# Kernel optimization log

Hardware: AMD Instinct MI355X
Metric: run time of the kernel (lower is better)

Reference implementation:

```python
import jax, jax.numpy as jnp
import numpy as np

N = 50000   # nodes
E = 800000  # directed edges (self loops added in reference)
F = 8       # temporal features
D = 64      # hidden_channels
H = 4       # heads
C = D // H  # per-head channels = 16
L = 3       # num GAT layers
T = 3       # node types
TE = 16     # type embed dim


def _glorot(key, shape):
    fan_in, fan_out = shape[-2], shape[-1]
    s = jnp.sqrt(6.0 / (fan_in + fan_out))
    return jax.random.uniform(key, shape, jnp.float32, -s, s)


def setup_inputs() -> dict:
    key = jax.random.key(0)
    ks = jax.random.split(key, 24)
    return {
        'x': jax.random.normal(ks[0], (N, F), jnp.float32),
        'node_type': jax.random.randint(ks[1], (N,), 0, T),
        'edge_src': jax.random.randint(ks[2], (E,), 0, N),
        'edge_dst': jax.random.randint(ks[3], (E,), 0, N),
        # TemporalEncoder (Linear F->D + ReLU)
        'Wt': _glorot(ks[4], (F, D)), 'bt': jnp.zeros((D,), jnp.float32),
        # type embedding and input projection
        'Et': 0.1 * jax.random.normal(ks[5], (T, TE), jnp.float32),
        'Wp': _glorot(ks[6], (D + TE, D)), 'bp': jnp.zeros((D,), jnp.float32),
        # GATv2 layers (stacked over L)
        'Wl': _glorot(ks[7], (L, D, H * C)), 'bl': jnp.zeros((L, H * C), jnp.float32),
        'Wr': _glorot(ks[8], (L, D, H * C)), 'br': jnp.zeros((L, H * C), jnp.float32),
        'att': _glorot(ks[9], (L, H, C)),
        'Wres': _glorot(ks[10], (L, D, H * C)),
        'bconv': jnp.zeros((L, H * C), jnp.float32),
        'gamma': jnp.ones((L, D), jnp.float32), 'beta': jnp.zeros((L, D), jnp.float32),
        'alpha': jnp.float32(0.5),
        # output head
        'W1': _glorot(ks[11], (D, D // 2)), 'b1': jnp.zeros((D // 2,), jnp.float32),
        'W2': _glorot(ks[12], (D // 2, 1)), 'b2': jnp.zeros((1,), jnp.float32),
    }


def _layernorm(x, g, b, eps=1e-5):
    mu = jnp.mean(x, -1, keepdims=True)
    v = jnp.mean((x - mu) ** 2, -1, keepdims=True)
    return g * (x - mu) / jnp.sqrt(v + eps) + b


def reference(x, node_type, edge_src, edge_dst, Wt, bt, Et, Wp, bp,
              Wl, bl, Wr, br, att, Wres, bconv, gamma, beta, alpha,
              W1, b1, W2, b2):
    # temporal encoder + type embedding + input projection
    h = jax.nn.relu(x @ Wt + bt)                       # [N, D]
    h = jnp.concatenate([h, Et[node_type]], axis=-1) @ Wp + bp
    h0 = h

    # add self loops once (eval mode -> no dropout)
    loop = jnp.arange(N)
    src = jnp.concatenate([edge_src, loop])            # [E']
    dst = jnp.concatenate([edge_dst, loop])

    for l in range(L):
        xl = (h @ Wl[l] + bl[l]).reshape(N, H, C)      # source transform
        xr = (h @ Wr[l] + br[l]).reshape(N, H, C)      # target transform
        e = jax.nn.leaky_relu(xl[src] + xr[dst], 0.2)  # [E', H, C]
        score = jnp.einsum('ehc,hc->eh', e, att[l])    # [E', H]
        # segment softmax over incoming edges of each destination node
        m = jax.ops.segment_max(score, dst, num_segments=N)
        ex = jnp.exp(score - m[dst])
        s = jax.ops.segment_sum(ex, dst, num_segments=N)
        a = ex / (s[dst] + 1e-16)                      # [E', H]
        msg = xl[src] * a[:, :, None]                  # [E', H, C]
        out = jax.ops.segment_sum(msg, dst, num_segments=N).reshape(N, H * C)
        out = out + h @ Wres[l] + bconv[l]             # GATv2 residual + bias
        h = _layernorm(alpha * out + (1.0 - alpha) * h0, gamma[l], beta[l])

    z = jax.nn.relu(h @ W1 + b1)
    return jax.nn.sigmoid(z @ W2 + b2)                 # [N, 1]
```

## Files before the change

### kernel.cpp

```cpp
#include <hip/hip_runtime.h>
#include <hip/hip_bf16.h>

typedef __hip_bfloat16 bf16;
typedef __attribute__((ext_vector_type(8))) short short8;
typedef __attribute__((ext_vector_type(4))) float f32x4;

__device__ __forceinline__ float b2f(bf16 v) { return __bfloat162float(v); }
__device__ __forceinline__ bf16 f2b(float v) { return __float2bfloat16(v); }
__device__ __forceinline__ short f2bs(float v) {
    bf16 b = f2b(v);
    return *reinterpret_cast<short*>(&b);
}
__device__ __forceinline__ float bflo(unsigned int u) { return __uint_as_float(u << 16); }
__device__ __forceinline__ float bfhi(unsigned int u) { return __uint_as_float(u & 0xffff0000u); }
__device__ __forceinline__ unsigned int packbf(float lo, float hi) {
    bf16 l = f2b(lo), h = f2b(hi);
    return ((unsigned int)(*(unsigned short*)&h) << 16) | (*(unsigned short*)&l);
}


__global__ void k_sentinel(float* out, int n, float val) {
    int i = blockIdx.x * blockDim.x + threadIdx.x;
    if (i < n) out[i] = val;
}

__global__ void k_prep(const float* __restrict__ Wl, const float* __restrict__ Wr,
                       const float* __restrict__ Wres, const float* __restrict__ Wp,
                       const float* __restrict__ W1, const float* __restrict__ Et,
                       const float* __restrict__ bp,
                       bf16* __restrict__ WT, bf16* __restrict__ WpT,
                       bf16* __restrict__ W1T, float* __restrict__ TyB,
                       int* __restrict__ counts, int n) {
    int i = blockIdx.x * 256 + threadIdx.x;
    if (i < n) counts[i] = 0;
    if (i < 36864) {
        int l = i / 12288, rem = i % 12288;
        int col = rem / 64, k = rem % 64;
        int mat = col >> 6, c = col & 63;
        const float* W = (mat == 0) ? Wl : (mat == 1) ? Wr : Wres;
        WT[i] = f2b(W[l * 4096 + k * 64 + c]);
    } else if (i < 40960) {
        int j = i - 36864, col = j / 64, k = j % 64;
        WpT[j] = f2b(Wp[k * 64 + col]);
    } else if (i < 43008) {
        int j = i - 40960, col = j / 64, k = j % 64;
        W1T[j] = f2b(W1[k * 32 + col]);
    } else if (i < 43200) {
        int j = i - 43008, t = j / 64, d = j % 64;
        float s = bp[d];
#pragma unroll
        for (int f = 0; f < 16; ++f) s += Et[t * 16 + f] * Wp[(64 + f) * 64 + d];
        TyB[j] = s;
    }
}

__global__ __launch_bounds__(256) void k_enc_mfma(
        const float* __restrict__ x, const int* __restrict__ ntype,
        const float* __restrict__ Wt, const float* __restrict__ bt,
        const bf16* __restrict__ WpT, const float* __restrict__ TyB,
        float* __restrict__ h0, bf16* __restrict__ hbf, int n) {
    __shared__ float sWt[512];
    __shared__ float sbt[64];
    int tid = threadIdx.x;
    for (int i = tid; i < 512; i += 256) sWt[i] = Wt[i];
    if (tid < 64) sbt[tid] = bt[tid];
    __syncthreads();
    int wave = tid >> 6, lane = tid & 63;
    int nb = blockIdx.x * 64 + wave * 16;
    if (nb >= n) return;
    int m = lane & 15, q = lane >> 4;

    const float* xrow = x + (size_t)(nb + m) * 8;
    float xv[8];
#pragma unroll
    for (int f = 0; f < 8; ++f) xv[f] = xrow[f];

    short8 a0, a1;
#pragma unroll
    for (int j = 0; j < 8; ++j) {
        int c0 = q * 8 + j, c1 = 32 + q * 8 + j;
        float s0 = sbt[c0], s1 = sbt[c1];
#pragma unroll
        for (int f = 0; f < 8; ++f) {
            s0 += xv[f] * sWt[f * 64 + c0];
            s1 += xv[f] * sWt[f * 64 + c1];
        }
        a0[j] = f2bs(fmaxf(s0, 0.f));
        a1[j] = f2bs(fmaxf(s1, 0.f));
    }

    int ty[4];
#pragma unroll
    for (int r = 0; r < 4; ++r) ty[r] = ntype[nb + q * 4 + r];

#pragma unroll
    for (int t = 0; t < 4; ++t) {
        const short* wp = (const short*)(WpT + (size_t)(t * 16 + m) * 64) + q * 8;
        short8 b0 = *(const short8*)(wp);
        short8 b1 = *(const short8*)(wp + 32);
        f32x4 acc = {0.f, 0.f, 0.f, 0.f};
        acc = __builtin_amdgcn_mfma_f32_16x16x32_bf16(a0, b0, acc, 0, 0, 0);
        acc = __builtin_amdgcn_mfma_f32_16x16x32_bf16(a1, b1, acc, 0, 0, 0);
        int col = t * 16 + m;
#pragma unroll
        for (int r = 0; r < 4; ++r) {
            int nd = nb + q * 4 + r;
            float val = acc[r] + TyB[ty[r] * 64 + col];
            h0[(size_t)nd * 64 + col] = val;
            hbf[(size_t)nd * 64 + col] = f2b(val);
        }
    }
}

__global__ void k_count(const int* __restrict__ dst, int* __restrict__ counts,
                        int* __restrict__ rank, int e) {
    int i = blockIdx.x * blockDim.x + threadIdx.x;
    if (i < e) rank[i] = atomicAdd(&counts[dst[i]], 1);
}

__global__ void k_scan_local(const int* __restrict__ counts, int* __restrict__ row_raw,
                             int* __restrict__ bsum, int n) {
    __shared__ int part[256];
    int tid = threadIdx.x;
    int base = blockIdx.x * 1024 + tid * 4;
    int c0 = (base     < n) ? counts[base]     + 1 : 0;
    int c1 = (base + 1 < n) ? counts[base + 1] + 1 : 0;
    int c2 = (base + 2 < n) ? counts[base + 2] + 1 : 0;
    int c3 = (base + 3 < n) ? counts[base + 3] + 1 : 0;
    part[tid] = c0 + c1 + c2 + c3;
    __syncthreads();
    for (int off = 1; off < 256; off <<= 1) {
        int t = (tid >= off) ? part[tid - off] : 0;
        __syncthreads();
        part[tid] += t;
        __syncthreads();
    }
    int ex = (tid == 0) ? 0 : part[tid - 1];
    if (base     < n) row_raw[base]     = ex;
    if (base + 1 < n) row_raw[base + 1] = ex + c0;
    if (base + 2 < n) row_raw[base + 2] = ex + c0 + c1;
    if (base + 3 < n) row_raw[base + 3] = ex + c0 + c1 + c2;
    if (tid == 255) bsum[blockIdx.x] = part[255];
}

__global__ void k_scan_bsum(int* __restrict__ bsum, int* __restrict__ row_ptr,
                            int g, int n) {
    int lane = threadIdx.x;
    int orig = (lane < g) ? bsum[lane] : 0;
    int v = orig;
#pragma unroll
    for (int off = 1; off < 64; off <<= 1) {
        int t = __shfl_up(v, off, 64);
        if (lane >= off) v += t;
    }
    if (lane < g) bsum[lane] = v - orig;
    if (lane == 63) row_ptr[n] = v;
}

__global__ void k_build(const int* __restrict__ src, const int* __restrict__ dst,
                        const int* __restrict__ row_raw, const int* __restrict__ bsum,
                        const int* __restrict__ rank,
                        int* __restrict__ row_ptr, int* __restrict__ csr_src,
                        int n, int e) {
    int i = blockIdx.x * 256 + threadIdx.x;
    if (i < n) {
        int rp = row_raw[i] + bsum[i >> 10];
        row_ptr[i] = rp;
        csr_src[rp] = i;
    }
    if (i < e) {
        int d = dst[i];
        int pos = row_raw[d] + bsum[d >> 10] + 1 + rank[i];
        csr_src[pos] = src[i];
    }
}

__global__ __launch_bounds__(256) void k_xform_mfma(
        const bf16* __restrict__ hbf, const bf16* __restrict__ WT,
        const float* __restrict__ bl, const float* __restrict__ br,
        const float* __restrict__ bconv,
        bf16* __restrict__ xl, bf16* __restrict__ xr, bf16* __restrict__ res, int n) {
    int wave = threadIdx.x >> 6, lane = threadIdx.x & 63;
    int nb = blockIdx.x * 64 + wave * 16;
    if (nb >= n) return;
    int m = lane & 15, q = lane >> 4;

    const short* hrow = (const short*)(hbf + (size_t)(nb + m) * 64) + q * 8;
    short8 a0 = *(const short8*)(hrow);
    short8 a1 = *(const short8*)(hrow + 32);

#pragma unroll
    for (int t = 0; t < 12; ++t) {
        const short* wp = (const short*)(WT + (size_t)(t * 16 + m) * 64) + q * 8;
        short8 b0 = *(const short8*)(wp);
        short8 b1 = *(const short8*)(wp + 32);
        f32x4 acc = {0.f, 0.f, 0.f, 0.f};
        acc = __builtin_amdgcn_mfma_f32_16x16x32_bf16(a0, b0, acc, 0, 0, 0);
        acc = __builtin_amdgcn_mfma_f32_16x16x32_bf16(a1, b1, acc, 0, 0, 0);

        int col = t * 16 + m;
        int mat = col >> 6, c = col & 63;
        float bias = (mat == 0) ? bl[c] : (mat == 1) ? br[c] : bconv[c];
        bf16* dst = (mat == 0) ? xl : (mat == 1) ? xr : res;
#pragma unroll
        for (int r = 0; r < 4; ++r)
            dst[(size_t)(nb + q * 4 + r) * 64 + c] = f2b(acc[r] + bias);
    }
}

#define GAT2_STEP(E_IDX, LS, A0S, A1S)                                            \
    {                                                                             \
        int s_ = csr_src[E_IDX];                                                  \
        unsigned int xu_ = *(const unsigned int*)((const unsigned short*)xl +     \
                                                  (size_t)s_ * 64 + ch);          \
        float x0_ = bflo(xu_), x1_ = bfhi(xu_);                                   \
        float t0_ = x0_ + xr0; t0_ = fmaxf(t0_, 0.2f * t0_);                      \
        float t1_ = x1_ + xr1; t1_ = fmaxf(t1_, 0.2f * t1_);                      \
        float p_ = t0_ * at0 + t1_ * at1;                                         \
        p_ += __shfl_xor(p_, 1, 64);                                              \
        p_ += __shfl_xor(p_, 2, 64);                                              \
        p_ += __shfl_xor(p_, 4, 64);                                              \
        float pe_ = __expf(fminf(p_, 60.f));                                      \
        A0S += pe_ * x0_;  A1S += pe_ * x1_;  LS += pe_;                          \
    }

__global__ __launch_bounds__(256) void k_gat(
        const bf16* __restrict__ xl, const bf16* __restrict__ xr,
        const bf16* __restrict__ res, const float* __restrict__ h0,
        const float* __restrict__ att, const float* __restrict__ gamma,
        const float* __restrict__ beta, const float* __restrict__ alpha_p,
        const int* __restrict__ row_ptr, const int* __restrict__ csr_src,
        bf16* __restrict__ hbf, int n) {
    int wave = threadIdx.x >> 6;
    int lane = threadIdx.x & 63;
    int half = lane >> 5;
    int L = lane & 31;
    int head = L >> 3, cp = L & 7;
    int ch = head * 16 + cp * 2;
    int v = (blockIdx.x * 4 + wave) * 2 + half;
    bool valid = v < n;
    int vv = valid ? v : 0;

    unsigned int xru = *(const unsigned int*)((const unsigned short*)xr +
                                              (size_t)vv * 64 + ch);
    float xr0 = bflo(xru), xr1 = bfhi(xru);
    float at0 = att[ch], at1 = att[ch + 1];

    int beg = row_ptr[vv];
    int end = valid ? row_ptr[vv + 1] : beg;

    float l0 = 0.f, A00 = 0.f, A01 = 0.f;
    float l1 = 0.f, A10 = 0.f, A11 = 0.f;
    int e = beg;
    for (; e + 1 < end; e += 2) {
        GAT2_STEP(e,     l0, A00, A01)
        GAT2_STEP(e + 1, l1, A10, A11)
    }
    if (e < end) GAT2_STEP(e, l0, A00, A01)

    float lsum = l0 + l1;
    float inv = 1.f / (lsum + 1e-16f);
    float acc0 = (A00 + A10) * inv;
    float acc1 = (A01 + A11) * inv;

    unsigned int ru = *(const unsigned int*)((const unsigned short*)res +
                                             (size_t)vv * 64 + ch);
    float o0 = acc0 + bflo(ru);
    float o1 = acc1 + bfhi(ru);
    float a = alpha_p[0];
    float t0 = a * o0 + (1.f - a) * h0[(size_t)vv * 64 + ch];
    float t1 = a * o1 + (1.f - a) * h0[(size_t)vv * 64 + ch + 1];

    float mu = t0 + t1;
#pragma unroll
    for (int o = 1; o < 32; o <<= 1) mu += __shfl_xor(mu, o, 64);
    mu *= (1.f / 64.f);
    float d0 = t0 - mu, d1 = t1 - mu;
    float var = d0 * d0 + d1 * d1;
#pragma unroll
    for (int o = 1; o < 32; o <<= 1) var += __shfl_xor(var, o, 64);
    var *= (1.f / 64.f);
    float rs = rsqrtf(var + 1e-5f);
    float hn0 = gamma[ch] * d0 * rs + beta[ch];
    float hn1 = gamma[ch + 1] * d1 * rs + beta[ch + 1];
    if (valid)
        *(unsigned int*)((unsigned short*)hbf + (size_t)v * 64 + ch) = packbf(hn0, hn1);
}

__global__ __launch_bounds__(256) void k_head_mfma(
        const bf16* __restrict__ hbf, const bf16* __restrict__ W1T,
        const float* __restrict__ b1, const float* __restrict__ W2,
        const float* __restrict__ b2, float* __restrict__ out, int n) {
    int wave = threadIdx.x >> 6, lane = threadIdx.x & 63;
    int nb = blockIdx.x * 64 + wave * 16;
    if (nb >= n) return;
    int m = lane & 15, q = lane >> 4;

    const short* hrow = (const short*)(hbf + (size_t)(nb + m) * 64) + q * 8;
    short8 a0 = *(const short8*)(hrow);
    short8 a1 = *(const short8*)(hrow + 32);

    const short* w0p = (const short*)(W1T + (size_t)m * 64) + q * 8;
    const short* w1p = (const short*)(W1T + (size_t)(16 + m) * 64) + q * 8;
    short8 b00 = *(const short8*)(w0p);
    short8 b01 = *(const short8*)(w0p + 32);
    short8 b10 = *(const short8*)(w1p);
    short8 b11 = *(const short8*)(w1p + 32);

    f32x4 acc0 = {0.f, 0.f, 0.f, 0.f};
    f32x4 acc1 = {0.f, 0.f, 0.f, 0.f};
    acc0 = __builtin_amdgcn_mfma_f32_16x16x32_bf16(a0, b00, acc0, 0, 0, 0);
    acc0 = __builtin_amdgcn_mfma_f32_16x16x32_bf16(a1, b01, acc0, 0, 0, 0);
    acc1 = __builtin_amdgcn_mfma_f32_16x16x32_bf16(a0, b10, acc1, 0, 0, 0);
    acc1 = __builtin_amdgcn_mfma_f32_16x16x32_bf16(a1, b11, acc1, 0, 0, 0);

    float w2a = W2[m], w2b = W2[16 + m];
    float bb0 = b1[m], bb1 = b1[16 + m];
    float part[4];
#pragma unroll
    for (int r = 0; r < 4; ++r)
        part[r] = fmaxf(acc0[r] + bb0, 0.f) * w2a + fmaxf(acc1[r] + bb1, 0.f) * w2b;
#pragma unroll
    for (int mask = 1; mask < 16; mask <<= 1) {
#pragma unroll
        for (int r = 0; r < 4; ++r) part[r] += __shfl_xor(part[r], mask, 64);
    }
    if (m == 0) {
        float bb2 = b2[0];
#pragma unroll
        for (int r = 0; r < 4; ++r)
            out[nb + q * 4 + r] = 1.f / (1.f + __expf(-(part[r] + bb2)));
    }
}

extern "C" void kernel_launch(void* const* d_in, const int* in_sizes, int n_in,
                              void* d_out, int out_size, void* d_ws, size_t ws_size,
                              hipStream_t stream) {
    const float* x     = (const float*)d_in[0];
    const int*   ntype = (const int*)d_in[1];
    const int*   esrc  = (const int*)d_in[2];
    const int*   edst  = (const int*)d_in[3];
    const float* Wt    = (const float*)d_in[4];
    const float* bt    = (const float*)d_in[5];
    const float* Et    = (const float*)d_in[6];
    const float* Wp    = (const float*)d_in[7];
    const float* bp    = (const float*)d_in[8];
    const float* Wl    = (const float*)d_in[9];
    const float* bl    = (const float*)d_in[10];
    const float* Wr    = (const float*)d_in[11];
    const float* br    = (const float*)d_in[12];
    const float* att   = (const float*)d_in[13];
    const float* Wres  = (const float*)d_in[14];
    const float* bconv = (const float*)d_in[15];
    const float* gamma = (const float*)d_in[16];
    const float* beta  = (const float*)d_in[17];
    const float* alpha = (const float*)d_in[18];
    const float* W1    = (const float*)d_in[19];
    const float* b1    = (const float*)d_in[20];
    const float* W2    = (const float*)d_in[21];
    const float* b2    = (const float*)d_in[22];
    float* out = (float*)d_out;

    const int N = in_sizes[1];
    const int E = in_sizes[2];

    const int G = (N + 1023) / 1024;

    size_t need = 256
                + (size_t)N * 64 * 4
                + (size_t)N * 64 * 2 * 4
                + (size_t)36864 * 2
                + (size_t)4096 * 2
                + (size_t)2048 * 2
                + (size_t)192 * 4
                + (size_t)N * 4
                + (size_t)(N + 1) * 4
                + (size_t)N * 4
                + (size_t)E * 4
                + 256
                + (size_t)(E + N) * 4;

    if (ws_size < need) {
        k_sentinel<<<(N + 255) / 256, 256, 0, stream>>>(out, N,
                                                        100.0f + (float)(ws_size >> 20));
        return;
    }

    char* ws = (char*)d_ws;
    ws += 256;
    float* h0   = (float*)ws; ws += (size_t)N * 64 * 4;
    bf16* hbf   = (bf16*)ws;  ws += (size_t)N * 64 * 2;
    bf16* xl    = (bf16*)ws;  ws += (size_t)N * 64 * 2;
    bf16* xr    = (bf16*)ws;  ws += (size_t)N * 64 * 2;
    bf16* res   = (bf16*)ws;  ws += (size_t)N * 64 * 2;
    bf16* WT    = (bf16*)ws;  ws += (size_t)36864 * 2;
    bf16* WpT   = (bf16*)ws;  ws += (size_t)4096 * 2;
    bf16* W1T   = (bf16*)ws;  ws += (size_t)2048 * 2;
    float* TyB  = (float*)ws; ws += (size_t)192 * 4;
    int* row_raw = (int*)ws;  ws += (size_t)N * 4;
    int* row_ptr = (int*)ws;  ws += (size_t)(N + 1) * 4;
    int* counts  = (int*)ws;  ws += (size_t)N * 4;
    int* rank    = (int*)ws;  ws += (size_t)E * 4;
    int* bsum    = (int*)ws;  ws += 256;
    int* csr_src = (int*)ws;  ws += (size_t)(E + N) * 4;

    int prepN = (N > 43200) ? N : 43200;
    k_prep<<<(prepN + 255) / 256, 256, 0, stream>>>(Wl, Wr, Wres, Wp, W1, Et, bp,
                                                    WT, WpT, W1T, TyB, counts, N);
    k_enc_mfma<<<(N + 63) / 64, 256, 0, stream>>>(x, ntype, Wt, bt, WpT, TyB,
                                                  h0, hbf, N);

    k_count<<<(E + 255) / 256, 256, 0, stream>>>(edst, counts, rank, E);
    k_scan_local<<<G, 256, 0, stream>>>(counts, row_raw, bsum, N);
    k_scan_bsum<<<1, 64, 0, stream>>>(bsum, row_ptr, G, N);
    k_build<<<(E + 255) / 256, 256, 0, stream>>>(esrc, edst, row_raw, bsum, rank,
                                                 row_ptr, csr_src, N, E);

    for (int l = 0; l < 3; ++l) {
        size_t bo = (size_t)l * 64;
        k_xform_mfma<<<(N + 63) / 64, 256, 0, stream>>>(
            hbf, WT + (size_t)l * 192 * 64,
            bl + bo, br + bo, bconv + bo, xl, xr, res, N);
        k_gat<<<(N + 7) / 8, 256, 0, stream>>>(xl, xr, res, h0,
                                               att + bo, gamma + bo, beta + bo, alpha,
                                               row_ptr, csr_src, hbf, N);
    }

    k_head_mfma<<<(N + 63) / 64, 256, 0, stream>>>(hbf, W1T, b1, W2, b2, out, N);
}
```

Before: 355.9 us.

## Fuse GAT layers with next-layer transforms and head, ping-pong feature buffers

Folds each layer's xl/xr/res projection into the preceding GAT aggregation kernel: normalized rows go to shared memory and are multiplied with MFMA, and xl/xr/res are double-buffered between layers. The encoder also computes the first layer's projections, and the output head is fused into the last GAT kernel. The edge counting is merged into the weight-prep kernel, counts are cleared with a memset, h0 is stored in bf16, and the edge loop is unrolled by four. This removes several launches and the hbf round trips through global memory. The cost is more shared-memory staging, 512-thread blocks with idle waves during the small matmul, and reduced h0 precision.

Measured after the change: 321.2 us. 9.7% less time.

```diff
diff --git a/kernel.cpp b/kernel.cpp
--- a/kernel.cpp
+++ b/kernel.cpp
@@ -24,43 +24,55 @@
     if (i < n) out[i] = val;
 }
 
-__global__ void k_prep(const float* __restrict__ Wl, const float* __restrict__ Wr,
-                       const float* __restrict__ Wres, const float* __restrict__ Wp,
-                       const float* __restrict__ W1, const float* __restrict__ Et,
-                       const float* __restrict__ bp,
-                       bf16* __restrict__ WT, bf16* __restrict__ WpT,
-                       bf16* __restrict__ W1T, float* __restrict__ TyB,
-                       int* __restrict__ counts, int n) {
-    int i = blockIdx.x * 256 + threadIdx.x;
-    if (i < n) counts[i] = 0;
-    if (i < 36864) {
-        int l = i / 12288, rem = i % 12288;
-        int col = rem / 64, k = rem % 64;
-        int mat = col >> 6, c = col & 63;
-        const float* W = (mat == 0) ? Wl : (mat == 1) ? Wr : Wres;
-        WT[i] = f2b(W[l * 4096 + k * 64 + c]);
-    } else if (i < 40960) {
-        int j = i - 36864, col = j / 64, k = j % 64;
-        WpT[j] = f2b(Wp[k * 64 + col]);
-    } else if (i < 43008) {
-        int j = i - 40960, col = j / 64, k = j % 64;
-        W1T[j] = f2b(W1[k * 32 + col]);
-    } else if (i < 43200) {
-        int j = i - 43008, t = j / 64, d = j % 64;
-        float s = bp[d];
-#pragma unroll
-        for (int f = 0; f < 16; ++f) s += Et[t * 16 + f] * Wp[(64 + f) * 64 + d];
-        TyB[j] = s;
-    }
-}
-
-__global__ __launch_bounds__(256) void k_enc_mfma(
+#define PREP_BLOCKS 169
+__global__ void k_setup(const float* __restrict__ Wl, const float* __restrict__ Wr,
+                        const float* __restrict__ Wres, const float* __restrict__ Wp,
+                        const float* __restrict__ W1, const float* __restrict__ Et,
+                        const float* __restrict__ bp,
+                        bf16* __restrict__ WT, bf16* __restrict__ WpT,
+                        bf16* __restrict__ W1T, float* __restrict__ TyB,
+                        const int* __restrict__ edst, int* __restrict__ counts,
+                        int* __restrict__ rank, int e) {
+    int b = blockIdx.x;
+    if (b < PREP_BLOCKS) {
+        int i = b * 256 + threadIdx.x;
+        if (i < 36864) {
+            int l = i / 12288, rem = i % 12288;
+            int col = rem / 64, k = rem % 64;
+            int mat = col >> 6, c = col & 63;
+            const float* W = (mat == 0) ? Wl : (mat == 1) ? Wr : Wres;
+            WT[i] = f2b(W[l * 4096 + k * 64 + c]);
+        } else if (i < 40960) {
+            int j = i - 36864, col = j / 64, k = j % 64;
+            WpT[j] = f2b(Wp[k * 64 + col]);
+        } else if (i < 43008) {
+            int j = i - 40960, col = j / 64, k = j % 64;
+            W1T[j] = f2b(W1[k * 32 + col]);
+        } else if (i < 43200) {
+            int j = i - 43008, t = j / 64, d = j % 64;
+            float s = bp[d];
+#pragma unroll
+            for (int f = 0; f < 16; ++f) s += Et[t * 16 + f] * Wp[(64 + f) * 64 + d];
+            TyB[j] = s;
+        }
+    } else {
+        int i = (b - PREP_BLOCKS) * 256 + threadIdx.x;
+        if (i < e) rank[i] = atomicAdd(&counts[edst[i]], 1);
+    }
+}
+
+__global__ __launch_bounds__(256) void k_encx(
         const float* __restrict__ x, const int* __restrict__ ntype,
         const float* __restrict__ Wt, const float* __restrict__ bt,
         const bf16* __restrict__ WpT, const float* __restrict__ TyB,
-        float* __restrict__ h0, bf16* __restrict__ hbf, int n) {
+        bf16* __restrict__ h0b,
+        const bf16* __restrict__ WT0, const float* __restrict__ bl0,
+        const float* __restrict__ br0, const float* __restrict__ bc0,
+        bf16* __restrict__ xlo, bf16* __restrict__ xro, bf16* __restrict__ reso,
+        int n) {
     __shared__ float sWt[512];
     __shared__ float sbt[64];
+    __shared__ __align__(16) short sh[4 * 16 * 72];
     int tid = threadIdx.x;
     for (int i = tid; i < 512; i += 256) sWt[i] = Wt[i];
     if (tid < 64) sbt[tid] = bt[tid];
@@ -69,6 +81,7 @@
     int nb = blockIdx.x * 64 + wave * 16;
     if (nb >= n) return;
     int m = lane & 15, q = lane >> 4;
+    short* shw = sh + wave * 16 * 72;
 
     const float* xrow = x + (size_t)(nb + m) * 8;
     float xv[8];
@@ -105,17 +118,29 @@
 #pragma unroll
         for (int r = 0; r < 4; ++r) {
             int nd = nb + q * 4 + r;
-            float val = acc[r] + TyB[ty[r] * 64 + col];
-            h0[(size_t)nd * 64 + col] = val;
-            hbf[(size_t)nd * 64 + col] = f2b(val);
-        }
-    }
-}
-
-__global__ void k_count(const int* __restrict__ dst, int* __restrict__ counts,
-                        int* __restrict__ rank, int e) {
-    int i = blockIdx.x * blockDim.x + threadIdx.x;
-    if (i < e) rank[i] = atomicAdd(&counts[dst[i]], 1);
+            short vb = f2bs(acc[r] + TyB[ty[r] * 64 + col]);
+            h0b[(size_t)nd * 64 + col] = *reinterpret_cast<bf16*>(&vb);
+            shw[(q * 4 + r) * 72 + col] = vb;
+        }
+    }
+    short8 ha0 = *(const short8*)(&shw[m * 72 + q * 8]);
+    short8 ha1 = *(const short8*)(&shw[m * 72 + 32 + q * 8]);
+#pragma unroll
+    for (int t = 0; t < 12; ++t) {
+        const short* wp = (const short*)(WT0 + (size_t)(t * 16 + m) * 64) + q * 8;
+        short8 b0 = *(const short8*)(wp);
+        short8 b1 = *(const short8*)(wp + 32);
+        f32x4 acc = {0.f, 0.f, 0.f, 0.f};
+        acc = __builtin_amdgcn_mfma_f32_16x16x32_bf16(ha0, b0, acc, 0, 0, 0);
+        acc = __builtin_amdgcn_mfma_f32_16x16x32_bf16(ha1, b1, acc, 0, 0, 0);
+        int col = t * 16 + m;
+        int mat = col >> 6, c = col & 63;
+        float bias = (mat == 0) ? bl0[c] : (mat == 1) ? br0[c] : bc0[c];
+        bf16* dst = (mat == 0) ? xlo : (mat == 1) ? xro : reso;
+#pragma unroll
+        for (int r = 0; r < 4; ++r)
+            dst[(size_t)(nb + q * 4 + r) * 64 + c] = f2b(acc[r] + bias);
+    }
 }
 
 __global__ void k_scan_local(const int* __restrict__ counts, int* __restrict__ row_raw,
@@ -175,39 +200,6 @@
     }
 }
 
-__global__ __launch_bounds__(256) void k_xform_mfma(
-        const bf16* __restrict__ hbf, const bf16* __restrict__ WT,
-        const float* __restrict__ bl, const float* __restrict__ br,
-        const float* __restrict__ bconv,
-        bf16* __restrict__ xl, bf16* __restrict__ xr, bf16* __restrict__ res, int n) {
-    int wave = threadIdx.x >> 6, lane = threadIdx.x & 63;
-    int nb = blockIdx.x * 64 + wave * 16;
-    if (nb >= n) return;
-    int m = lane & 15, q = lane >> 4;
-
-    const short* hrow = (const short*)(hbf + (size_t)(nb + m) * 64) + q * 8;
-    short8 a0 = *(const short8*)(hrow);
-    short8 a1 = *(const short8*)(hrow + 32);
-
-#pragma unroll
-    for (int t = 0; t < 12; ++t) {
-        const short* wp = (const short*)(WT + (size_t)(t * 16 + m) * 64) + q * 8;
-        short8 b0 = *(const short8*)(wp);
-        short8 b1 = *(const short8*)(wp + 32);
-        f32x4 acc = {0.f, 0.f, 0.f, 0.f};
-        acc = __builtin_amdgcn_mfma_f32_16x16x32_bf16(a0, b0, acc, 0, 0, 0);
-        acc = __builtin_amdgcn_mfma_f32_16x16x32_bf16(a1, b1, acc, 0, 0, 0);
-
-        int col = t * 16 + m;
-        int mat = col >> 6, c = col & 63;
-        float bias = (mat == 0) ? bl[c] : (mat == 1) ? br[c] : bconv[c];
-        bf16* dst = (mat == 0) ? xl : (mat == 1) ? xr : res;
-#pragma unroll
-        for (int r = 0; r < 4; ++r)
-            dst[(size_t)(nb + q * 4 + r) * 64 + c] = f2b(acc[r] + bias);
-    }
-}
-
 #define GAT2_STEP(E_IDX, LS, A0S, A1S)                                            \
     {                                                                             \
         int s_ = csr_src[E_IDX];                                                  \
@@ -224,112 +216,153 @@
         A0S += pe_ * x0_;  A1S += pe_ * x1_;  LS += pe_;                          \
     }
 
-__global__ __launch_bounds__(256) void k_gat(
+#define GAT_PHASE_BODY                                                            \
+    int tid = threadIdx.x;                                                        \
+    int wave = tid >> 6, lane = tid & 63;                                         \
+    int half = lane >> 5;                                                         \
+    int L = lane & 31;                                                            \
+    int head = L >> 3, cp = L & 7;                                                \
+    int ch = head * 16 + cp * 2;                                                  \
+    int nl = wave * 2 + half;                                                     \
+    int v = blockIdx.x * 16 + nl;                                                 \
+    bool valid = v < n;                                                           \
+    int vv = valid ? v : 0;                                                       \
+    unsigned int xru = *(const unsigned int*)((const unsigned short*)xr +         \
+                                              (size_t)vv * 64 + ch);              \
+    float xr0 = bflo(xru), xr1 = bfhi(xru);                                       \
+    float at0 = att[ch], at1 = att[ch + 1];                                       \
+    int beg = row_ptr[vv];                                                        \
+    int end = valid ? row_ptr[vv + 1] : beg;                                      \
+    float l0 = 0.f, A00 = 0.f, A01 = 0.f;                                         \
+    float l1 = 0.f, A10 = 0.f, A11 = 0.f;                                         \
+    float l2 = 0.f, A20 = 0.f, A21 = 0.f;                                         \
+    float l3 = 0.f, A30 = 0.f, A31 = 0.f;                                         \
+    int e = beg;                                                                  \
+    for (; e + 3 < end; e += 4) {                                                 \
+        GAT2_STEP(e,     l0, A00, A01)                                            \
+        GAT2_STEP(e + 1, l1, A10, A11)                                            \
+        GAT2_STEP(e + 2, l2, A20, A21)                                            \
+        GAT2_STEP(e + 3, l3, A30, A31)                                            \
+    }                                                                             \
+    int rem = end - e;                                                            \
+    if (rem > 0) GAT2_STEP(e,     l0, A00, A01)                                   \
+    if (rem > 1) GAT2_STEP(e + 1, l1, A10, A11)                                   \
+    if (rem > 2) GAT2_STEP(e + 2, l2, A20, A21)                                   \
+    float lsum = (l0 + l1) + (l2 + l3);                                           \
+    float inv = 1.f / (lsum + 1e-16f);                                            \
+    float acc0 = ((A00 + A10) + (A20 + A30)) * inv;                               \
+    float acc1 = ((A01 + A11) + (A21 + A31)) * inv;                               \
+    unsigned int ru = *(const unsigned int*)((const unsigned short*)res +         \
+                                             (size_t)vv * 64 + ch);               \
+    unsigned int hu = *(const unsigned int*)((const unsigned short*)h0b +         \
+                                             (size_t)vv * 64 + ch);               \
+    float o0 = acc0 + bflo(ru);                                                   \
+    float o1 = acc1 + bfhi(ru);                                                   \
+    float a = alpha_p[0];                                                         \
+    float t0 = a * o0 + (1.f - a) * bflo(hu);                                     \
+    float t1 = a * o1 + (1.f - a) * bfhi(hu);                                     \
+    float mu = t0 + t1;                                                           \
+    _Pragma("unroll")                                                             \
+    for (int o = 1; o < 32; o <<= 1) mu += __shfl_xor(mu, o, 64);                 \
+    mu *= (1.f / 64.f);                                                           \
+    float d0 = t0 - mu, d1 = t1 - mu;                                             \
+    float var = d0 * d0 + d1 * d1;                                                \
+    _Pragma("unroll")                                                             \
+    for (int o = 1; o < 32; o <<= 1) var += __shfl_xor(var, o, 64);               \
+    var *= (1.f / 64.f);                                                          \
+    float rs = rsqrtf(var + 1e-5f);                                               \
+    float hn0 = gamma[ch] * d0 * rs + beta[ch];                                   \
+    float hn1 = gamma[ch + 1] * d1 * rs + beta[ch + 1];                           \
+    *(unsigned int*)((char*)sh + nl * 144 + ch * 2) = packbf(hn0, hn1);           \
+    __syncthreads();
+
+__global__ __launch_bounds__(512) void k_gatx(
         const bf16* __restrict__ xl, const bf16* __restrict__ xr,
-        const bf16* __restrict__ res, const float* __restrict__ h0,
+        const bf16* __restrict__ res, const bf16* __restrict__ h0b,
         const float* __restrict__ att, const float* __restrict__ gamma,
         const float* __restrict__ beta, const float* __restrict__ alpha_p,
         const int* __restrict__ row_ptr, const int* __restrict__ csr_src,
-        bf16* __restrict__ hbf, int n) {
-    int wave = threadIdx.x >> 6;
-    int lane = threadIdx.x & 63;
-    int half = lane >> 5;
-    int L = lane & 31;
-    int head = L >> 3, cp = L & 7;
-    int ch = head * 16 + cp * 2;
-    int v = (blockIdx.x * 4 + wave) * 2 + half;
-    bool valid = v < n;
-    int vv = valid ? v : 0;
-
-    unsigned int xru = *(const unsigned int*)((const unsigned short*)xr +
-                                              (size_t)vv * 64 + ch);
-    float xr0 = bflo(xru), xr1 = bfhi(xru);
-    float at0 = att[ch], at1 = att[ch + 1];
-
-    int beg = row_ptr[vv];
-    int end = valid ? row_ptr[vv + 1] : beg;
-
-    float l0 = 0.f, A00 = 0.f, A01 = 0.f;
-    float l1 = 0.f, A10 = 0.f, A11 = 0.f;
-    int e = beg;
-    for (; e + 1 < end; e += 2) {
-        GAT2_STEP(e,     l0, A00, A01)
-        GAT2_STEP(e + 1, l1, A10, A11)
-    }
-    if (e < end) GAT2_STEP(e, l0, A00, A01)
-
-    float lsum = l0 + l1;
-    float inv = 1.f / (lsum + 1e-16f);
-    float acc0 = (A00 + A10) * inv;
-    float acc1 = (A01 + A11) * inv;
-
-    unsigned int ru = *(const unsigned int*)((const unsigned short*)res +
-                                             (size_t)vv * 64 + ch);
-    float o0 = acc0 + bflo(ru);
-    float o1 = acc1 + bfhi(ru);
-    float a = alpha_p[0];
-    float t0 = a * o0 + (1.f - a) * h0[(size_t)vv * 64 + ch];
-    float t1 = a * o1 + (1.f - a) * h0[(size_t)vv * 64 + ch + 1];
-
-    float mu = t0 + t1;
-#pragma unroll
-    for (int o = 1; o < 32; o <<= 1) mu += __shfl_xor(mu, o, 64);
-    mu *= (1.f / 64.f);
-    float d0 = t0 - mu, d1 = t1 - mu;
-    float var = d0 * d0 + d1 * d1;
-#pragma unroll
-    for (int o = 1; o < 32; o <<= 1) var += __shfl_xor(var, o, 64);
-    var *= (1.f / 64.f);
-    float rs = rsqrtf(var + 1e-5f);
-    float hn0 = gamma[ch] * d0 * rs + beta[ch];
-    float hn1 = gamma[ch + 1] * d1 * rs + beta[ch + 1];
-    if (valid)
-        *(unsigned int*)((unsigned short*)hbf + (size_t)v * 64 + ch) = packbf(hn0, hn1);
-}
-
-__global__ __launch_bounds__(256) void k_head_mfma(
-        const bf16* __restrict__ hbf, const bf16* __restrict__ W1T,
-        const float* __restrict__ b1, const float* __restrict__ W2,
-        const float* __restrict__ b2, float* __restrict__ out, int n) {
-    int wave = threadIdx.x >> 6, lane = threadIdx.x & 63;
-    int nb = blockIdx.x * 64 + wave * 16;
-    if (nb >= n) return;
+        const bf16* __restrict__ WTn, const float* __restrict__ bln,
+        const float* __restrict__ brn, const float* __restrict__ bcn,
+        bf16* __restrict__ xlo, bf16* __restrict__ xro, bf16* __restrict__ reso,
+        int n) {
+    __shared__ __align__(16) short sh[16 * 72];
+    GAT_PHASE_BODY
+
     int m = lane & 15, q = lane >> 4;
-
-    const short* hrow = (const short*)(hbf + (size_t)(nb + m) * 64) + q * 8;
-    short8 a0 = *(const short8*)(hrow);
-    short8 a1 = *(const short8*)(hrow + 32);
-
-    const short* w0p = (const short*)(W1T + (size_t)m * 64) + q * 8;
-    const short* w1p = (const short*)(W1T + (size_t)(16 + m) * 64) + q * 8;
-    short8 b00 = *(const short8*)(w0p);
-    short8 b01 = *(const short8*)(w0p + 32);
-    short8 b10 = *(const short8*)(w1p);
-    short8 b11 = *(const short8*)(w1p + 32);
-
-    f32x4 acc0 = {0.f, 0.f, 0.f, 0.f};
-    f32x4 acc1 = {0.f, 0.f, 0.f, 0.f};
-    acc0 = __builtin_amdgcn_mfma_f32_16x16x32_bf16(a0, b00, acc0, 0, 0, 0);
-    acc0 = __builtin_amdgcn_mfma_f32_16x16x32_bf16(a1, b01, acc0, 0, 0, 0);
-    acc1 = __builtin_amdgcn_mfma_f32_16x16x32_bf16(a0, b10, acc1, 0, 0, 0);
-    acc1 = __builtin_amdgcn_mfma_f32_16x16x32_bf16(a1, b11, acc1, 0, 0, 0);
-
-    float w2a = W2[m], w2b = W2[16 + m];
-    float bb0 = b1[m], bb1 = b1[16 + m];
-    float part[4];
-#pragma unroll
-    for (int r = 0; r < 4; ++r)
-        part[r] = fmaxf(acc0[r] + bb0, 0.f) * w2a + fmaxf(acc1[r] + bb1, 0.f) * w2b;
-#pragma unroll
-    for (int mask = 1; mask < 16; mask <<= 1) {
-#pragma unroll
-        for (int r = 0; r < 4; ++r) part[r] += __shfl_xor(part[r], mask, 64);
-    }
-    if (m == 0) {
-        float bb2 = b2[0];
+    short8 ha0 = *(const short8*)(&sh[m * 72 + q * 8]);
+    short8 ha1 = *(const short8*)(&sh[m * 72 + 32 + q * 8]);
+    int nb = blockIdx.x * 16;
+    for (int t = wave; t < 12; t += 8) {
+        const short* wp = (const short*)(WTn + (size_t)(t * 16 + m) * 64) + q * 8;
+        short8 b0 = *(const short8*)(wp);
+        short8 b1 = *(const short8*)(wp + 32);
+        f32x4 acc = {0.f, 0.f, 0.f, 0.f};
+        acc = __builtin_amdgcn_mfma_f32_16x16x32_bf16(ha0, b0, acc, 0, 0, 0);
+        acc = __builtin_amdgcn_mfma_f32_16x16x32_bf16(ha1, b1, acc, 0, 0, 0);
+        int col = t * 16 + m;
+        int mat = col >> 6, c = col & 63;
+        float bias = (mat == 0) ? bln[c] : (mat == 1) ? brn[c] : bcn[c];
+        bf16* dst = (mat == 0) ? xlo : (mat == 1) ? xro : reso;
+#pragma unroll
+        for (int r = 0; r < 4; ++r) {
+            int nd = nb + q * 4 + r;
+            if (nd < n) dst[(size_t)nd * 64 + c] = f2b(acc[r] + bias);
+        }
+    }
+}
+
+__global__ __launch_bounds__(512) void k_gath(
+        const bf16* __restrict__ xl, const bf16* __restrict__ xr,
+        const bf16* __restrict__ res, const bf16* __restrict__ h0b,
+        const float* __restrict__ att, const float* __restrict__ gamma,
+        const float* __restrict__ beta, const float* __restrict__ alpha_p,
+        const int* __restrict__ row_ptr, const int* __restrict__ csr_src,
+        const bf16* __restrict__ W1T, const float* __restrict__ b1,
+        const float* __restrict__ W2, const float* __restrict__ b2,
+        float* __restrict__ out, int n) {
+    __shared__ __align__(16) short sh[16 * 72];
+    GAT_PHASE_BODY
+
+    if (wave == 0) {
+        int m = lane & 15, q = lane >> 4;
+        short8 ha0 = *(const short8*)(&sh[m * 72 + q * 8]);
+        short8 ha1 = *(const short8*)(&sh[m * 72 + 32 + q * 8]);
+
+        const short* w0p = (const short*)(W1T + (size_t)m * 64) + q * 8;
+        const short* w1p = (const short*)(W1T + (size_t)(16 + m) * 64) + q * 8;
+        short8 b00 = *(const short8*)(w0p);
+        short8 b01 = *(const short8*)(w0p + 32);
+        short8 b10 = *(const short8*)(w1p);
+        short8 b11 = *(const short8*)(w1p + 32);
+
+        f32x4 acc0 = {0.f, 0.f, 0.f, 0.f};
+        f32x4 acc1 = {0.f, 0.f, 0.f, 0.f};
+        acc0 = __builtin_amdgcn_mfma_f32_16x16x32_bf16(ha0, b00, acc0, 0, 0, 0);
+        acc0 = __builtin_amdgcn_mfma_f32_16x16x32_bf16(ha1, b01, acc0, 0, 0, 0);
+        acc1 = __builtin_amdgcn_mfma_f32_16x16x32_bf16(ha0, b10, acc1, 0, 0, 0);
+        acc1 = __builtin_amdgcn_mfma_f32_16x16x32_bf16(ha1, b11, acc1, 0, 0, 0);
+
+        float w2a = W2[m], w2b = W2[16 + m];
+        float bb0 = b1[m], bb1 = b1[16 + m];
+        float part[4];
 #pragma unroll
         for (int r = 0; r < 4; ++r)
-            out[nb + q * 4 + r] = 1.f / (1.f + __expf(-(part[r] + bb2)));
+            part[r] = fmaxf(acc0[r] + bb0, 0.f) * w2a + fmaxf(acc1[r] + bb1, 0.f) * w2b;
+#pragma unroll
+        for (int mask = 1; mask < 16; mask <<= 1) {
+#pragma unroll
+            for (int r = 0; r < 4; ++r) part[r] += __shfl_xor(part[r], mask, 64);
+        }
+        if (m == 0) {
+            float bb2 = b2[0];
+            int nb = blockIdx.x * 16;
+#pragma unroll
+            for (int r = 0; r < 4; ++r) {
+                int nd = nb + q * 4 + r;
+                if (nd < n) out[nd] = 1.f / (1.f + __expf(-(part[r] + bb2)));
+            }
+        }
     }
 }
 
@@ -367,11 +400,8 @@
     const int G = (N + 1023) / 1024;
 
     size_t need = 256
-                + (size_t)N * 64 * 4
-                + (size_t)N * 64 * 2 * 4
-                + (size_t)36864 * 2
-                + (size_t)4096 * 2
-                + (size_t)2048 * 2
+                + (size_t)N * 64 * 2 * 7
+                + (size_t)36864 * 2 + (size_t)4096 * 2 + (size_t)2048 * 2
                 + (size_t)192 * 4
                 + (size_t)N * 4
                 + (size_t)(N + 1) * 4
@@ -388,11 +418,13 @@
 
     char* ws = (char*)d_ws;
     ws += 256;
-    float* h0   = (float*)ws; ws += (size_t)N * 64 * 4;
-    bf16* hbf   = (bf16*)ws;  ws += (size_t)N * 64 * 2;
-    bf16* xl    = (bf16*)ws;  ws += (size_t)N * 64 * 2;
-    bf16* xr    = (bf16*)ws;  ws += (size_t)N * 64 * 2;
-    bf16* res   = (bf16*)ws;  ws += (size_t)N * 64 * 2;
+    bf16* h0b   = (bf16*)ws;  ws += (size_t)N * 64 * 2;
+    bf16* xlA   = (bf16*)ws;  ws += (size_t)N * 64 * 2;
+    bf16* xrA   = (bf16*)ws;  ws += (size_t)N * 64 * 2;
+    bf16* resA  = (bf16*)ws;  ws += (size_t)N * 64 * 2;
+    bf16* xlB   = (bf16*)ws;  ws += (size_t)N * 64 * 2;
+    bf16* xrB   = (bf16*)ws;  ws += (size_t)N * 64 * 2;
+    bf16* resB  = (bf16*)ws;  ws += (size_t)N * 64 * 2;
     bf16* WT    = (bf16*)ws;  ws += (size_t)36864 * 2;
     bf16* WpT   = (bf16*)ws;  ws += (size_t)4096 * 2;
     bf16* W1T   = (bf16*)ws;  ws += (size_t)2048 * 2;
@@ -404,27 +436,23 @@
     int* bsum    = (int*)ws;  ws += 256;
     int* csr_src = (int*)ws;  ws += (size_t)(E + N) * 4;
 
-    int prepN = (N > 43200) ? N : 43200;
-    k_prep<<<(prepN + 255) / 256, 256, 0, stream>>>(Wl, Wr, Wres, Wp, W1, Et, bp,
-                                                    WT, WpT, W1T, TyB, counts, N);
-    k_enc_mfma<<<(N + 63) / 64, 256, 0, stream>>>(x, ntype, Wt, bt, WpT, TyB,
-                                                  h0, hbf, N);
-
-    k_count<<<(E + 255) / 256, 256, 0, stream>>>(edst, counts, rank, E);
+    hipMemsetAsync(counts, 0, (size_t)N * 4, stream);
+    k_setup<<<PREP_BLOCKS + (E + 255) / 256, 256, 0, stream>>>(
+        Wl, Wr, Wres, Wp, W1, Et, bp, WT, WpT, W1T, TyB, edst, counts, rank, E);
+    k_encx<<<(N + 63) / 64, 256, 0, stream>>>(x, ntype, Wt, bt, WpT, TyB, h0b,
+                                              WT, bl, br, bconv, xlA, xrA, resA, N);
     k_scan_local<<<G, 256, 0, stream>>>(counts, row_raw, bsum, N);
     k_scan_bsum<<<1, 64, 0, stream>>>(bsum, row_ptr, G, N);
     k_build<<<(E + 255) / 256, 256, 0, stream>>>(esrc, edst, row_raw, bsum, rank,
                                                  row_ptr, csr_src, N, E);
 
-    for (int l = 0; l < 3; ++l) {
-        size_t bo = (size_t)l * 64;
-        k_xform_mfma<<<(N + 63) / 64, 256, 0, stream>>>(
-            hbf, WT + (size_t)l * 192 * 64,
-            bl + bo, br + bo, bconv + bo, xl, xr, res, N);
-        k_gat<<<(N + 7) / 8, 256, 0, stream>>>(xl, xr, res, h0,
-                                               att + bo, gamma + bo, beta + bo, alpha,
-                                               row_ptr, csr_src, hbf, N);
-    }
-
-    k_head_mfma<<<(N + 63) / 64, 256, 0, stream>>>(hbf, W1T, b1, W2, b2, out, N);
-}
+    k_gatx<<<(N + 15) / 16, 512, 0, stream>>>(
+        xlA, xrA, resA, h0b, att, gamma, beta, alpha, row_ptr, csr_src,
+        WT + 12288, bl + 64, br + 64, bconv + 64, xlB, xrB, resB, N);
+    k_gatx<<<(N + 15) / 16, 512, 0, stream>>>(
+        xlB, xrB, resB, h0b, att + 64, gamma + 64, beta + 64, alpha, row_ptr, csr_src,
+        WT + 24576, bl + 128, br + 128, bconv + 128, xlA, xrA, resA, N);
+    k_gath<<<(N + 15) / 16, 512, 0, stream>>>(
+        xlA, xrA, resA, h0b, att + 128, gamma + 128, beta + 128, alpha,
+        row_ptr, csr_src, W1T, b1, W2, b2, out, N);
+}
```
